# Optimization experiments

Measured on AMD Instinct MI355X. Metric: run time of the kernel, lower is better.

The kernel has to match this reference:

```python
import jax, jax.numpy as jnp
import numpy as np

EPS = 1e-5

def conv1d(x, w, b, pad):
    # x: (N,C,L), w: (O,I,K) torch layout
    y = jax.lax.conv_general_dilated(x, w, (1,), [(pad, pad)],
                                     dimension_numbers=('NCH', 'OIH', 'NCH'))
    return y + b[None, :, None]

def convT1d(x, w, b, stride, pad):
    # torch ConvTranspose1d; w: (I,O,K) torch layout
    K = w.shape[-1]
    wt = jnp.flip(w, -1).transpose(1, 0, 2)  # (O,I,K)
    y = jax.lax.conv_general_dilated(x, wt, (1,), [(K - 1 - pad, K - 1 - pad)],
                                     lhs_dilation=(stride,),
                                     dimension_numbers=('NCH', 'OIH', 'NCH'))
    return y + b[None, :, None]

def batchnorm1d(x, g, b):
    # training-mode batch stats over (N, L) per channel
    m = jnp.mean(x, axis=(0, 2), keepdims=True)
    v = jnp.var(x, axis=(0, 2), keepdims=True)
    return (x - m) * jax.lax.rsqrt(v + EPS) * g[None, :, None] + b[None, :, None]

def maxpool2(x):
    N, C, L = x.shape
    L2 = (L // 2) * 2
    return x[:, :, :L2].reshape(N, C, L // 2, 2).max(-1)

def linear(x, w, b):
    return x @ w.T + b

def gcn_conv(x, src, dst, w, b, n_nodes):
    # PyG GCNConv: add self-loops, symmetric norm, linear, aggregate
    h = x @ w.T  # (N, out)
    loop = jnp.arange(n_nodes, dtype=src.dtype)
    s = jnp.concatenate([src, loop])
    d = jnp.concatenate([dst, loop])
    deg = jax.ops.segment_sum(jnp.ones_like(d, dtype=h.dtype), d, num_segments=n_nodes)
    dinv = jax.lax.rsqrt(jnp.maximum(deg, 1e-12))
    norm = dinv[s] * dinv[d]  # (E+N,)
    msg = h[s] * norm[:, None]
    out = jax.ops.segment_sum(msg, d, num_segments=n_nodes)
    return out + b

def _params(key):
    ks = jax.random.split(key, 32)
    i = iter(range(32))
    def w(shape, k):
        return jax.random.normal(k, shape, dtype=jnp.float32) * 0.05
    F = 2944  # 128 * (187 // 8)
    p = {}
    p['ec1_w'] = w((32, 1, 5), ks[next(i)]);   p['ec1_b'] = jnp.zeros(32)
    p['bn1e_g'] = jnp.ones(32);                p['bn1e_b'] = jnp.zeros(32)
    p['ec2_w'] = w((64, 32, 5), ks[next(i)]);  p['ec2_b'] = jnp.zeros(64)
    p['bn2e_g'] = jnp.ones(64);                p['bn2e_b'] = jnp.zeros(64)
    p['ec3_w'] = w((128, 64, 5), ks[next(i)]); p['ec3_b'] = jnp.zeros(128)
    p['bn3e_g'] = jnp.ones(128);               p['bn3e_b'] = jnp.zeros(128)
    p['efc1_w'] = w((256, F), ks[next(i)]);    p['efc1_b'] = jnp.zeros(256)
    p['efc2_w'] = w((128, 256), ks[next(i)]);  p['efc2_b'] = jnp.zeros(128)
    p['g1_w'] = w((128, 128), ks[next(i)]);    p['g1_b'] = jnp.zeros(128)
    p['g2_w'] = w((128, 128), ks[next(i)]);    p['g2_b'] = jnp.zeros(128)
    p['c1_w'] = w((64, 128), ks[next(i)]);     p['c1_b'] = jnp.zeros(64)
    p['c2_w'] = w((5, 64), ks[next(i)]);       p['c2_b'] = jnp.zeros(5)
    p['cls_emb'] = w((5, 32), ks[next(i)])
    p['dfc1_w'] = w((256, 160), ks[next(i)]);  p['dfc1_b'] = jnp.zeros(256)
    p['dfc2_w'] = w((F, 256), ks[next(i)]);    p['dfc2_b'] = jnp.zeros(F)
    p['dc1_w'] = w((128, 64, 4), ks[next(i)]); p['dc1_b'] = jnp.zeros(64)
    p['bn1d_g'] = jnp.ones(64);                p['bn1d_b'] = jnp.zeros(64)
    p['dc2_w'] = w((64, 32, 4), ks[next(i)]);  p['dc2_b'] = jnp.zeros(32)
    p['bn2d_g'] = jnp.ones(32);                p['bn2d_b'] = jnp.zeros(32)
    p['dc3_w'] = w((32, 1, 4), ks[next(i)]);   p['dc3_b'] = jnp.zeros(1)
    return p

def setup_inputs() -> dict:
    key = jax.random.key(0)
    k1, k2, k3, kp = jax.random.split(key, 4)
    N, E = 20000, 640000
    inp = {
        'waveforms': jax.random.normal(k1, (N, 1, 187), dtype=jnp.float32),
        'edge_index': jax.random.randint(k2, (2, E), 0, N, dtype=jnp.int64)
                      if jax.config.jax_enable_x64 else
                      jax.random.randint(k2, (2, E), 0, N, dtype=jnp.int32),
        'class_labels': jax.random.randint(k3, (N,), 0, 5, dtype=jnp.int32),
    }
    inp.update(_params(kp))
    return inp

def _forward(waveforms, edge_index, class_labels, p):
    N = waveforms.shape[0]
    # ---- ECGEncoder ----
    x = maxpool2(jax.nn.relu(batchnorm1d(conv1d(waveforms, p['ec1_w'], p['ec1_b'], 2), p['bn1e_g'], p['bn1e_b'])))
    x = maxpool2(jax.nn.relu(batchnorm1d(conv1d(x, p['ec2_w'], p['ec2_b'], 2), p['bn2e_g'], p['bn2e_b'])))
    x = maxpool2(jax.nn.relu(batchnorm1d(conv1d(x, p['ec3_w'], p['ec3_b'], 2), p['bn3e_g'], p['bn3e_b'])))
    x = x.reshape(N, -1)  # (N, 2944)
    x = jax.nn.relu(linear(x, p['efc1_w'], p['efc1_b']))  # dropout = identity (eval)
    feats = linear(x, p['efc2_w'], p['efc2_b'])  # (N, 128)
    # ---- GCNEncoder ----
    src, dst = edge_index[0], edge_index[1]
    h = jax.nn.relu(gcn_conv(feats, src, dst, p['g1_w'], p['g1_b'], N))
    z = gcn_conv(h, src, dst, p['g2_w'], p['g2_b'], N)
    # ---- Classifier ----
    logits = linear(jax.nn.relu(linear(z, p['c1_w'], p['c1_b'])), p['c2_w'], p['c2_b'])
    # ---- ClassConditionedDecoder ----
    emb = p['cls_emb'][class_labels]  # (N, 32)
    d = jnp.concatenate([z, emb], axis=1)  # (N, 160)
    d = jax.nn.relu(linear(d, p['dfc1_w'], p['dfc1_b']))
    d = jax.nn.relu(linear(d, p['dfc2_w'], p['dfc2_b']))
    d = d.reshape(N, 128, 23)
    d = jax.nn.relu(batchnorm1d(convT1d(d, p['dc1_w'], p['dc1_b'], 2, 1), p['bn1d_g'], p['bn1d_b']))  # (N,64,46)
    d = jax.nn.relu(batchnorm1d(convT1d(d, p['dc2_w'], p['dc2_b'], 2, 1), p['bn2d_g'], p['bn2d_b']))  # (N,32,92)
    d = convT1d(d, p['dc3_w'], p['dc3_b'], 2, 1)  # (N,1,184)
    recon = jnp.pad(d, ((0, 0), (0, 0), (0, 187 - d.shape[2])))
    return z, recon, logits

PARAM_NAMES = ['ec1_w','ec1_b','bn1e_g','bn1e_b','ec2_w','ec2_b','bn2e_g','bn2e_b','ec3_w','ec3_b','bn3e_g','bn3e_b','efc1_w','efc1_b','efc2_w','efc2_b','g1_w','g1_b','g2_w','g2_b','c1_w','c1_b','c2_w','c2_b','cls_emb','dfc1_w','dfc1_b','dfc2_w','dfc2_b','dc1_w','dc1_b','bn1d_g','bn1d_b','dc2_w','dc2_b','bn2d_g','bn2d_b','dc3_w','dc3_b']

def reference(waveforms, edge_index, class_labels,
              ec1_w, ec1_b, bn1e_g, bn1e_b, ec2_w, ec2_b, bn2e_g, bn2e_b,
              ec3_w, ec3_b, bn3e_g, bn3e_b, efc1_w, efc1_b, efc2_w, efc2_b,
              g1_w, g1_b, g2_w, g2_b, c1_w, c1_b, c2_w, c2_b, cls_emb,
              dfc1_w, dfc1_b, dfc2_w, dfc2_b, dc1_w, dc1_b, bn1d_g, bn1d_b,
              dc2_w, dc2_b, bn2d_g, bn2d_b, dc3_w, dc3_b):
    p = dict(zip(PARAM_NAMES, (ec1_w, ec1_b, bn1e_g, bn1e_b, ec2_w, ec2_b, bn2e_g, bn2e_b,
                               ec3_w, ec3_b, bn3e_g, bn3e_b, efc1_w, efc1_b, efc2_w, efc2_b,
                               g1_w, g1_b, g2_w, g2_b, c1_w, c1_b, c2_w, c2_b, cls_emb,
                               dfc1_w, dfc1_b, dfc2_w, dfc2_b, dc1_w, dc1_b, bn1d_g, bn1d_b,
                               dc2_w, dc2_b, bn2d_g, bn2d_b, dc3_w, dc3_b)))
    return _forward(waveforms, edge_index, class_labels, p)
```

## Files before the change

kernel.cpp:

```cpp
#include <hip/hip_runtime.h>
#include <hip/hip_bf16.h>

using bf16 = __hip_bfloat16;

#define NS 20000
#define NE 640000
#define BN_EPS 1e-5f

__device__ __forceinline__ float bf2f(bf16 x) { return __bfloat162float(x); }
__device__ __forceinline__ bf16 f2bf(float x) { return __float2bfloat16(x); }
__device__ __forceinline__ float us2f(unsigned short u) { return __uint_as_float(((unsigned)u) << 16); }

__device__ __forceinline__ float4 load4f(const float* p) { return *reinterpret_cast<const float4*>(p); }
__device__ __forceinline__ void storeOut(float* p, float v) { *p = v; }
__device__ __forceinline__ void storeOut(bf16* p, float v) { *p = f2bf(v); }

__global__ __launch_bounds__(256) void k_wprep(const float* __restrict__ w2, const float* __restrict__ w3,
    float* __restrict__ W2T, bf16* __restrict__ W3T)
{
  int i = blockIdx.x * 256 + threadIdx.x;
  if (i < 10240) { int oc = i / 160, tap = i % 160; W2T[tap * 64 + oc] = w2[i]; }
  if (i < 40960) {
    int h = i / 20480, r = i % 20480;
    int oc = r / 320, tap = r % 320;
    W3T[h * 20480 + tap * 64 + oc] = f2bf(w3[i]);
  }
}

__global__ __launch_bounds__(256) void k_conv1_stats(const float* __restrict__ wav,
    const float* __restrict__ w1, const float* __restrict__ b1, float* __restrict__ stats)
{
  __shared__ float xs[192];
  __shared__ float ssum[32], ssq[32];
  int n = blockIdx.x, t = threadIdx.x;
  if (t < 187) xs[2 + t] = wav[n * 187 + t];
  else if (t == 187) { xs[0] = 0.f; xs[1] = 0.f; }
  else if (t == 188) { xs[189] = 0.f; xs[190] = 0.f; xs[191] = 0.f; }
  if (t < 32) { ssum[t] = 0.f; ssq[t] = 0.f; }
  __syncthreads();
  int c = t & 31, g = t >> 5;
  float wr[5];
#pragma unroll
  for (int k = 0; k < 5; ++k) wr[k] = w1[c * 5 + k];
  float bias = b1[c], s = 0.f, s2 = 0.f;
  for (int l = g; l < 187; l += 8) {
    float y = bias;
#pragma unroll
    for (int k = 0; k < 5; ++k) y = fmaf(xs[l + k], wr[k], y);
    s += y; s2 = fmaf(y, y, s2);
  }
  atomicAdd(&ssum[c], s); atomicAdd(&ssq[c], s2);
  __syncthreads();
  if (t < 32) { atomicAdd(&stats[t], ssum[t]); atomicAdd(&stats[128 + t], ssq[t]); }
}

__global__ void k_bn_finalize(float* __restrict__ stats, const float* __restrict__ g,
                              const float* __restrict__ b, int C, float invCnt, int off)
{
  int t = threadIdx.x;
  if (t < C) {
    float mean = stats[t] * invCnt;
    float var = stats[128 + t] * invCnt - mean * mean;
    float sc = g[t] * rsqrtf(var + BN_EPS);
    stats[off + t] = sc;
    stats[off + 128 + t] = b[t] - mean * sc;
  }
}

__global__ __launch_bounds__(256) void k_s2stats(const float* __restrict__ wav,
    const float* __restrict__ w1, const float* __restrict__ b1,
    const float* __restrict__ sc1, const float* __restrict__ sh1,
    const float* __restrict__ W2T, const float* __restrict__ b2,
    float* __restrict__ statacc)
{
  __shared__ float xs[192];
  __shared__ float p1[32 * 104];
  __shared__ __align__(16) float w2t[10240];
  __shared__ float ssum[64], ssq[64];
  int n = blockIdx.x, t = threadIdx.x;
  for (int i = t; i < 2560; i += 256)
    reinterpret_cast<float4*>(w2t)[i] = reinterpret_cast<const float4*>(W2T)[i];
  if (t < 187) xs[2 + t] = wav[n * 187 + t];
  else if (t == 187) { xs[0] = 0.f; xs[1] = 0.f; }
  else if (t == 188) { xs[189] = 0.f; xs[190] = 0.f; xs[191] = 0.f; }
  if (t < 64) { ssum[t] = 0.f; ssq[t] = 0.f; }
  if (t < 32) {
    p1[t * 104 + 0] = 0.f; p1[t * 104 + 1] = 0.f;
#pragma unroll
    for (int m = 95; m < 104; ++m) p1[t * 104 + m] = 0.f;
  }
  __syncthreads();
  {
    int c = t & 31, g = t >> 5;
    float wr[5];
#pragma unroll
    for (int k = 0; k < 5; ++k) wr[k] = w1[c * 5 + k];
    float bias = b1[c], sc = sc1[c], sh = sh1[c];
    for (int lp = g; lp < 93; lp += 8) {
      int b0 = 2 * lp;
      float y0 = bias, y1 = bias;
#pragma unroll
      for (int k = 0; k < 5; ++k) {
        y0 = fmaf(xs[b0 + k], wr[k], y0);
        y1 = fmaf(xs[b0 + 1 + k], wr[k], y1);
      }
      y0 = fmaf(y0, sc, sh); y1 = fmaf(y1, sc, sh);
      p1[c * 104 + 2 + lp] = fmaxf(fmaxf(y0, y1), 0.f);
    }
  }
  __syncthreads();
  int oc = (t & 15) * 4, l0 = (t >> 4) * 6;
  float acc[4][6] = {};
  for (int i = 0; i < 32; ++i) {
    float xv[10];
#pragma unroll
    for (int j = 0; j < 10; ++j) xv[j] = p1[i * 104 + l0 + j];
#pragma unroll
    for (int k = 0; k < 5; ++k) {
      const float4 wv = *reinterpret_cast<const float4*>(&w2t[(i * 5 + k) * 64 + oc]);
#pragma unroll
      for (int j = 0; j < 6; ++j) {
        acc[0][j] = fmaf(xv[j + k], wv.x, acc[0][j]);
        acc[1][j] = fmaf(xv[j + k], wv.y, acc[1][j]);
        acc[2][j] = fmaf(xv[j + k], wv.z, acc[2][j]);
        acc[3][j] = fmaf(xv[j + k], wv.w, acc[3][j]);
      }
    }
  }
#pragma unroll
  for (int c = 0; c < 4; ++c) {
    float bias = b2[oc + c], s = 0.f, s2 = 0.f;
#pragma unroll
    for (int j = 0; j < 6; ++j) {
      if (l0 + j < 93) {
        float y = acc[c][j] + bias;
        s += y; s2 = fmaf(y, y, s2);
      }
    }
    atomicAdd(&ssum[oc + c], s); atomicAdd(&ssq[oc + c], s2);
  }
  __syncthreads();
  if (t < 64) { atomicAdd(&statacc[t], ssum[t]); atomicAdd(&statacc[128 + t], ssq[t]); }
}

__global__ __launch_bounds__(256) void k_s123(const float* __restrict__ wav,
    const float* __restrict__ w1, const float* __restrict__ b1,
    const float* __restrict__ sc1, const float* __restrict__ sh1,
    const float* __restrict__ W2T, const float* __restrict__ b2,
    const float* __restrict__ sc2, const float* __restrict__ sh2,
    const bf16* __restrict__ W3T, const float* __restrict__ b3,
    bf16* __restrict__ praw3, float* __restrict__ statacc)
{
  __shared__ float xs[192];
  __shared__ float ssum[128], ssq[128];
  __shared__ __align__(16) char Rb[54272];
  float* p1  = (float*)Rb;
  float* w2t = (float*)(Rb + 13312);
  float* p2  = (float*)Rb;
  bf16*  w3t = (bf16*)(Rb + 13312);
  int n = blockIdx.x, t = threadIdx.x;
  for (int i = t; i < 2560; i += 256)
    reinterpret_cast<float4*>(w2t)[i] = reinterpret_cast<const float4*>(W2T)[i];
  if (t < 187) xs[2 + t] = wav[n * 187 + t];
  else if (t == 187) { xs[0] = 0.f; xs[1] = 0.f; }
  else if (t == 188) { xs[189] = 0.f; xs[190] = 0.f; xs[191] = 0.f; }
  if (t < 128) { ssum[t] = 0.f; ssq[t] = 0.f; }
  if (t < 32) {
    p1[t * 104 + 0] = 0.f; p1[t * 104 + 1] = 0.f;
#pragma unroll
    for (int m = 95; m < 104; ++m) p1[t * 104 + m] = 0.f;
  }
  __syncthreads();
  {
    int c = t & 31, g = t >> 5;
    float wr[5];
#pragma unroll
    for (int k = 0; k < 5; ++k) wr[k] = w1[c * 5 + k];
    float bias = b1[c], sc = sc1[c], sh = sh1[c];
    for (int lp = g; lp < 93; lp += 8) {
      int b0 = 2 * lp;
      float y0 = bias, y1 = bias;
#pragma unroll
      for (int k = 0; k < 5; ++k) {
        y0 = fmaf(xs[b0 + k], wr[k], y0);
        y1 = fmaf(xs[b0 + 1 + k], wr[k], y1);
      }
      y0 = fmaf(y0, sc, sh); y1 = fmaf(y1, sc, sh);
      p1[c * 104 + 2 + lp] = fmaxf(fmaxf(y0, y1), 0.f);
    }
  }
  __syncthreads();
  int oc = (t & 15) * 4, g2 = t >> 4, l0 = g2 * 6;
  float acc[4][6] = {};
  for (int i = 0; i < 32; ++i) {
    float xv[10];
#pragma unroll
    for (int j = 0; j < 10; ++j) xv[j] = p1[i * 104 + l0 + j];
#pragma unroll
    for (int k = 0; k < 5; ++k) {
      const float4 wv = *reinterpret_cast<const float4*>(&w2t[(i * 5 + k) * 64 + oc]);
#pragma unroll
      for (int j = 0; j < 6; ++j) {
        acc[0][j] = fmaf(xv[j + k], wv.x, acc[0][j]);
        acc[1][j] = fmaf(xv[j + k], wv.y, acc[1][j]);
        acc[2][j] = fmaf(xv[j + k], wv.z, acc[2][j]);
        acc[3][j] = fmaf(xv[j + k], wv.w, acc[3][j]);
      }
    }
  }
  __syncthreads();
#pragma unroll
  for (int c = 0; c < 4; ++c) {
    int ch = oc + c;
    float bias = b2[ch], sc = sc2[ch], sh = sh2[ch];
#pragma unroll
    for (int u = 0; u < 3; ++u) {
      int pp = 3 * g2 + u;
      if (pp < 46) {
        float ya = fmaf(acc[c][2 * u] + bias, sc, sh);
        float yb = fmaf(acc[c][2 * u + 1] + bias, sc, sh);
        p2[ch * 52 + 2 + pp] = fmaxf(fmaxf(ya, yb), 0.f);
      }
    }
  }
  if (t < 64) {
    p2[t * 52 + 0] = 0.f; p2[t * 52 + 1] = 0.f;
    p2[t * 52 + 48] = 0.f; p2[t * 52 + 49] = 0.f; p2[t * 52 + 50] = 0.f; p2[t * 52 + 51] = 0.f;
  }
  for (int h = 0; h < 2; ++h) {
    __syncthreads();
    for (int i = t; i < 10240; i += 256)
      reinterpret_cast<unsigned*>(w3t)[i] = reinterpret_cast<const unsigned*>(W3T + h * 20480)[i];
    __syncthreads();
    int oc2 = (t & 31) * 2, gb = t >> 5, l0b = gb * 6;
    float a2[2][6] = {};
    for (int i = 0; i < 64; ++i) {
      float xv[10];
#pragma unroll
      for (int j = 0; j < 10; ++j) xv[j] = p2[i * 52 + l0b + j];
#pragma unroll
      for (int k = 0; k < 5; ++k) {
        unsigned wp = *reinterpret_cast<const unsigned*>(&w3t[(i * 5 + k) * 64 + oc2]);
        float wa = us2f((unsigned short)(wp & 0xffffu));
        float wb = us2f((unsigned short)(wp >> 16));
#pragma unroll
        for (int j = 0; j < 6; ++j) {
          a2[0][j] = fmaf(xv[j + k], wa, a2[0][j]);
          a2[1][j] = fmaf(xv[j + k], wb, a2[1][j]);
        }
      }
    }
#pragma unroll
    for (int c = 0; c < 2; ++c) {
      int ch = h * 64 + oc2 + c;
      float bias3 = b3[ch], s = 0.f, s2 = 0.f;
      float yv[6];
#pragma unroll
      for (int j = 0; j < 6; ++j) {
        yv[j] = a2[c][j] + bias3;
        if (l0b + j < 46) { s += yv[j]; s2 = fmaf(yv[j], yv[j], s2); }
      }
#pragma unroll
      for (int u = 0; u < 3; ++u) {
        int pp = 3 * gb + u;
        if (pp < 23) praw3[(size_t)n * 2944 + ch * 23 + pp] = f2bf(fmaxf(yv[2 * u], yv[2 * u + 1]));
      }
      atomicAdd(&ssum[ch], s); atomicAdd(&ssq[ch], s2);
    }
  }
  __syncthreads();
  if (t < 128) { atomicAdd(&statacc[t], ssum[t]); atomicAdd(&statacc[128 + t], ssq[t]); }
}

__global__ __launch_bounds__(256) void k_efc1(const bf16* __restrict__ praw,
    const float* __restrict__ sc3, const float* __restrict__ sh3,
    const float* __restrict__ W, const float* __restrict__ bias, float* __restrict__ C)
{
  const int M = NS, K = 2944, O = 256;
  __shared__ float As[16][68];
  __shared__ float Bs[16][68];
  __shared__ float scs[128], shs[128];
  int tid = threadIdx.x;
  if (tid < 128) { scs[tid] = sc3[tid]; shs[tid] = sh3[tid]; }
  __syncthreads();
  int bm = blockIdx.x * 64, bo = blockIdx.y * 64;
  int lr = tid >> 2, lk = (tid & 3) * 4;
  int tm = (tid & 15) * 4, to = (tid >> 4) * 4;
  float acc[4][4] = {};
  for (int k0 = 0; k0 < K; k0 += 16) {
    float a0 = 0.f, a1 = 0.f, a2 = 0.f, a3 = 0.f;
    float4 wv = make_float4(0.f, 0.f, 0.f, 0.f);
    int arow = bm + lr;
    if (arow < M) {
      int kb = k0 + lk;
      ushort4 u4 = *reinterpret_cast<const ushort4*>(praw + (size_t)arow * K + kb);
      int c0 = (kb + 0) / 23, c1 = (kb + 1) / 23, c2 = (kb + 2) / 23, c3 = (kb + 3) / 23;
      a0 = fmaxf(fmaf(us2f(u4.x), scs[c0], shs[c0]), 0.f);
      a1 = fmaxf(fmaf(us2f(u4.y), scs[c1], shs[c1]), 0.f);
      a2 = fmaxf(fmaf(us2f(u4.z), scs[c2], shs[c2]), 0.f);
      a3 = fmaxf(fmaf(us2f(u4.w), scs[c3], shs[c3]), 0.f);
    }
    int orow = bo + lr;
    if (orow < O) wv = load4f(W + (size_t)orow * K + k0 + lk);
    As[lk + 0][lr] = a0; As[lk + 1][lr] = a1; As[lk + 2][lr] = a2; As[lk + 3][lr] = a3;
    Bs[lk + 0][lr] = wv.x; Bs[lk + 1][lr] = wv.y; Bs[lk + 2][lr] = wv.z; Bs[lk + 3][lr] = wv.w;
    __syncthreads();
#pragma unroll
    for (int k = 0; k < 16; ++k) {
      const float4 a = *reinterpret_cast<const float4*>(&As[k][tm]);
      const float4 b = *reinterpret_cast<const float4*>(&Bs[k][to]);
      float a4[4] = {a.x, a.y, a.z, a.w};
      float b4[4] = {b.x, b.y, b.z, b.w};
#pragma unroll
      for (int i = 0; i < 4; ++i)
#pragma unroll
        for (int j = 0; j < 4; ++j) acc[i][j] = fmaf(a4[i], b4[j], acc[i][j]);
    }
    __syncthreads();
  }
#pragma unroll
  for (int i = 0; i < 4; ++i) {
    int row = bm + tm + i;
    if (row >= M) continue;
#pragma unroll
    for (int j = 0; j < 4; ++j) {
      int col = bo + to + j;
      float v = acc[i][j] + bias[col];
      C[(size_t)row * O + col] = fmaxf(v, 0.f);
    }
  }
}

template <typename OT, bool RELU, bool RSCALE>
__global__ __launch_bounds__(256) void k_gemm(const float* __restrict__ A, const float* __restrict__ W,
    const float* __restrict__ bias, const float* __restrict__ rscale,
    OT* __restrict__ C, int M, int K, int O)
{
  __shared__ float As[16][68];
  __shared__ float Bs[16][68];
  int tid = threadIdx.x;
  int bm = blockIdx.x * 64, bo = blockIdx.y * 64;
  int lr = tid >> 2, lk = (tid & 3) * 4;
  int tm = (tid & 15) * 4, to = (tid >> 4) * 4;
  float acc[4][4] = {};
  for (int k0 = 0; k0 < K; k0 += 16) {
    float4 av = make_float4(0.f, 0.f, 0.f, 0.f);
    float4 wv = make_float4(0.f, 0.f, 0.f, 0.f);
    int arow = bm + lr;
    if (arow < M) av = load4f(A + (size_t)arow * K + k0 + lk);
    int orow = bo + lr;
    if (orow < O) wv = load4f(W + (size_t)orow * K + k0 + lk);
    As[lk + 0][lr] = av.x; As[lk + 1][lr] = av.y; As[lk + 2][lr] = av.z; As[lk + 3][lr] = av.w;
    Bs[lk + 0][lr] = wv.x; Bs[lk + 1][lr] = wv.y; Bs[lk + 2][lr] = wv.z; Bs[lk + 3][lr] = wv.w;
    __syncthreads();
#pragma unroll
    for (int k = 0; k < 16; ++k) {
      const float4 a = *reinterpret_cast<const float4*>(&As[k][tm]);
      const float4 b = *reinterpret_cast<const float4*>(&Bs[k][to]);
      float a4[4] = {a.x, a.y, a.z, a.w};
      float b4[4] = {b.x, b.y, b.z, b.w};
#pragma unroll
      for (int i = 0; i < 4; ++i)
#pragma unroll
        for (int j = 0; j < 4; ++j) acc[i][j] = fmaf(a4[i], b4[j], acc[i][j]);
    }
    __syncthreads();
  }
#pragma unroll
  for (int i = 0; i < 4; ++i) {
    int row = bm + tm + i;
    if (row >= M) continue;
    float rs = RSCALE ? rscale[row] : 1.f;
#pragma unroll
    for (int j = 0; j < 4; ++j) {
      int col = bo + to + j;
      if (col >= O) continue;
      float v = acc[i][j];
      if (bias) v += bias[col];
      if (RSCALE) v *= rs;
      if (RELU) v = fmaxf(v, 0.f);
      storeOut(&C[(size_t)row * O + col], v);
    }
  }
}

__global__ void k_degacc_int(const int* __restrict__ dst, int* __restrict__ dg)
{
  int e = blockIdx.x * 256 + threadIdx.x;
  if (e < NE) atomicAdd(&dg[dst[e]], 1);
}
__global__ __launch_bounds__(1024) void k_scan(const int* __restrict__ dg,
    int* __restrict__ off, int* __restrict__ cur)
{
  __shared__ int part[1024];
  int t = threadIdx.x;
  int base = t * 20;
  int local[20];
  int s = 0;
#pragma unroll
  for (int k = 0; k < 20; ++k) {
    int idx = base + k;
    int v = (idx < NS) ? dg[idx] : 0;
    local[k] = s; s += v;
  }
  part[t] = s;
  __syncthreads();
  for (int d = 1; d < 1024; d <<= 1) {
    int v = (t >= d) ? part[t - d] : 0;
    __syncthreads();
    part[t] += v;
    __syncthreads();
  }
  int pre = (t > 0) ? part[t - 1] : 0;
#pragma unroll
  for (int k = 0; k < 20; ++k) {
    int idx = base + k;
    if (idx < NS) { off[idx] = pre + local[k]; cur[idx] = pre + local[k]; }
  }
  if (t == 1023) off[NS] = part[1023];
}
__global__ void k_dinv(const int* __restrict__ dg, float* __restrict__ dinv)
{
  int i = blockIdx.x * 256 + threadIdx.x;
  if (i < NS) dinv[i] = rsqrtf((float)(dg[i] + 1));
}
__global__ void k_place(const int* __restrict__ src, const int* __restrict__ dst,
    int* __restrict__ cur, int* __restrict__ csr_src)
{
  int e = blockIdx.x * 256 + threadIdx.x;
  if (e < NE) {
    int p = atomicAdd(&cur[dst[e]], 1);
    csr_src[p] = src[e];
  }
}
template <bool RELU>
__global__ __launch_bounds__(128) void k_gcn_agg(const int* __restrict__ off,
    const int* __restrict__ csr_src, const float* __restrict__ hs,
    const float* __restrict__ dinv, const float* __restrict__ b, float* __restrict__ out)
{
  __shared__ int sidx[128];
  int n = blockIdx.x, t = threadIdx.x;
  int s0 = off[n], s1 = off[n + 1];
  float acc = 0.f;
  for (int base = s0; base < s1; base += 128) {
    int cnt = min(128, s1 - base);
    if (t < cnt) sidx[t] = csr_src[base + t];
    __syncthreads();
    for (int i = 0; i < cnt; ++i) acc += hs[(size_t)sidx[i] * 128 + t];
    __syncthreads();
  }
  float v = (acc + hs[(size_t)n * 128 + t]) * dinv[n] + b[t];
  if (RELU) v = fmaxf(v, 0.f);
  out[(size_t)n * 128 + t] = v;
}

__global__ void k_dcat(const float* __restrict__ z, const int* __restrict__ labels,
    const float* __restrict__ emb, float* __restrict__ dcat)
{
  int total = NS * 160;
  for (int i = blockIdx.x * 256 + threadIdx.x; i < total; i += gridDim.x * 256) {
    int n = i / 160, f = i % 160;
    dcat[i] = (f < 128) ? z[(size_t)n * 128 + f] : emb[labels[n] * 32 + (f - 128)];
  }
}

__global__ __launch_bounds__(256) void k_convT1(const bf16* __restrict__ d2,
    const float* __restrict__ w, const float* __restrict__ b,
    bf16* __restrict__ raw, float* __restrict__ stats)
{
  __shared__ float xsh[2944];
  __shared__ __align__(8) bf16 wsh[16384];
  __shared__ float ssum[64], ssq[64];
  int n = blockIdx.x, t = threadIdx.x;
  for (int i = t; i < 2944; i += 256) xsh[i] = bf2f(d2[(size_t)n * 2944 + i]);
  if (t < 64) { ssum[t] = 0.f; ssq[t] = 0.f; }
  int o = t & 63, g = t >> 6;
  float acc[12] = {};
  for (int half = 0; half < 2; ++half) {
    __syncthreads();
    for (int i = t; i < 16384; i += 256) wsh[i] = f2bf(w[half * 16384 + i]);
    __syncthreads();
    for (int i = 0; i < 64; ++i) {
      int ci = half * 64 + i;
      ushort4 w4 = *reinterpret_cast<const ushort4*>(&wsh[i * 256 + o * 4]);
      float w0 = us2f(w4.x), w1 = us2f(w4.y), w2v = us2f(w4.z), w3v = us2f(w4.w);
      float xl[8];
#pragma unroll
      for (int m = 0; m < 8; ++m) {
        int l = 6 * g - 1 + m;
        xl[m] = (l >= 0 && l < 23) ? xsh[ci * 23 + l] : 0.f;
      }
#pragma unroll
      for (int j = 0; j < 12; ++j) {
        if (j & 1) acc[j] = fmaf(w0, xl[(j + 1) / 2 + 1], fmaf(w2v, xl[(j + 1) / 2], acc[j]));
        else       acc[j] = fmaf(w1, xl[j / 2 + 1],       fmaf(w3v, xl[j / 2],       acc[j]));
      }
    }
  }
  float bias = b[o], s = 0.f, s2 = 0.f;
  size_t base = (size_t)n * 2944;
#pragma unroll
  for (int j = 0; j < 12; ++j) {
    int tp = 12 * g + j;
    if (tp < 46) {
      float y = acc[j] + bias;
      raw[base + (size_t)o * 46 + tp] = f2bf(y);
      s += y; s2 = fmaf(y, y, s2);
    }
  }
  atomicAdd(&ssum[o], s); atomicAdd(&ssq[o], s2);
  __syncthreads();
  if (t < 64) { atomicAdd(&stats[t], ssum[t]); atomicAdd(&stats[128 + t], ssq[t]); }
}

__global__ __launch_bounds__(256) void k_convT2(const bf16* __restrict__ raw1,
    const float* __restrict__ sc, const float* __restrict__ sh,
    const float* __restrict__ w, const float* __restrict__ b,
    bf16* __restrict__ raw2out, float* __restrict__ stats)
{
  __shared__ float xsh[2944];
  __shared__ __align__(16) float wsh[8192];
  __shared__ float ssum[32], ssq[32];
  int n = blockIdx.x, t = threadIdx.x;
  for (int i = t; i < 8192; i += 256) wsh[i] = w[i];
  for (int i = t; i < 2944; i += 256) {
    int c = i / 46;
    float v = fmaf(bf2f(raw1[(size_t)n * 2944 + i]), sc[c], sh[c]);
    xsh[i] = fmaxf(v, 0.f);
  }
  if (t < 32) { ssum[t] = 0.f; ssq[t] = 0.f; }
  __syncthreads();
  int o = t & 31, g = t >> 5;
  float acc[12] = {};
  for (int i = 0; i < 64; ++i) {
    const float4 wv = *reinterpret_cast<const float4*>(&wsh[i * 128 + o * 4]);
    float w0 = wv.x, w1 = wv.y, w2v = wv.z, w3v = wv.w;
    float xl[8];
#pragma unroll
    for (int m = 0; m < 8; ++m) {
      int l = 6 * g - 1 + m;
      xl[m] = (l >= 0 && l < 46) ? xsh[i * 46 + l] : 0.f;
    }
#pragma unroll
    for (int j = 0; j < 12; ++j) {
      if (j & 1) acc[j] = fmaf(w0, xl[(j + 1) / 2 + 1], fmaf(w2v, xl[(j + 1) / 2], acc[j]));
      else       acc[j] = fmaf(w1, xl[j / 2 + 1],       fmaf(w3v, xl[j / 2],       acc[j]));
    }
  }
  float bias = b[o], s = 0.f, s2 = 0.f;
  size_t base = (size_t)n * 2944;
#pragma unroll
  for (int j = 0; j < 12; ++j) {
    int tp = 12 * g + j;
    if (tp < 92) {
      float y = acc[j] + bias;
      raw2out[base + (size_t)o * 92 + tp] = f2bf(y);
      s += y; s2 = fmaf(y, y, s2);
    }
  }
  atomicAdd(&ssum[o], s); atomicAdd(&ssq[o], s2);
  __syncthreads();
  if (t < 32) { atomicAdd(&stats[t], ssum[t]); atomicAdd(&stats[128 + t], ssq[t]); }
}

__global__ __launch_bounds__(256) void k_convT3(const bf16* __restrict__ raw2,
    const float* __restrict__ sc, const float* __restrict__ sh,
    const float* __restrict__ w, const float* __restrict__ b,
    float* __restrict__ recon)
{
  __shared__ float xsh[2944];
  __shared__ float wsh[128];
  int n = blockIdx.x, t = threadIdx.x;
  if (t < 128) wsh[t] = w[t];
  for (int i = t; i < 2944; i += 256) {
    int c = i / 92;
    float v = fmaf(bf2f(raw2[(size_t)n * 2944 + i]), sc[c], sh[c]);
    xsh[i] = fmaxf(v, 0.f);
  }
  __syncthreads();
  if (t < 187) {
    float y = 0.f;
    if (t < 184) {
      y = b[0];
      if (t & 1) {
        int l1 = (t + 1) / 2, l2 = (t - 1) / 2;
        for (int i = 0; i < 32; ++i) {
          float a0 = (l1 < 92) ? wsh[i * 4 + 0] * xsh[i * 92 + l1] : 0.f;
          y += a0 + wsh[i * 4 + 2] * xsh[i * 92 + l2];
        }
      } else {
        int l1 = t / 2, l2 = t / 2 - 1;
        for (int i = 0; i < 32; ++i) {
          float a3 = (l2 >= 0) ? wsh[i * 4 + 3] * xsh[i * 92 + l2] : 0.f;
          y += wsh[i * 4 + 1] * xsh[i * 92 + l1] + a3;
        }
      }
    }
    recon[(size_t)n * 187 + t] = y;
  }
}

extern "C" void kernel_launch(void* const* d_in, const int* in_sizes, int n_in,
                              void* d_out, int out_size, void* d_ws, size_t ws_size,
                              hipStream_t stream)
{
  const float* wav    = (const float*)d_in[0];
  const int*   edges  = (const int*)d_in[1];
  const int*   labels = (const int*)d_in[2];
  int a = 3;
  const float* ec1_w = (const float*)d_in[a++]; const float* ec1_b = (const float*)d_in[a++];
  const float* bn1e_g = (const float*)d_in[a++]; const float* bn1e_b = (const float*)d_in[a++];
  const float* ec2_w = (const float*)d_in[a++]; const float* ec2_b = (const float*)d_in[a++];
  const float* bn2e_g = (const float*)d_in[a++]; const float* bn2e_b = (const float*)d_in[a++];
  const float* ec3_w = (const float*)d_in[a++]; const float* ec3_b = (const float*)d_in[a++];
  const float* bn3e_g = (const float*)d_in[a++]; const float* bn3e_b = (const float*)d_in[a++];
  const float* efc1_w = (const float*)d_in[a++]; const float* efc1_b = (const float*)d_in[a++];
  const float* efc2_w = (const float*)d_in[a++]; const float* efc2_b = (const float*)d_in[a++];
  const float* g1_w = (const float*)d_in[a++]; const float* g1_b = (const float*)d_in[a++];
  const float* g2_w = (const float*)d_in[a++]; const float* g2_b = (const float*)d_in[a++];
  const float* c1_w = (const float*)d_in[a++]; const float* c1_b = (const float*)d_in[a++];
  const float* c2_w = (const float*)d_in[a++]; const float* c2_b = (const float*)d_in[a++];
  const float* cls_emb = (const float*)d_in[a++];
  const float* dfc1_w = (const float*)d_in[a++]; const float* dfc1_b = (const float*)d_in[a++];
  const float* dfc2_w = (const float*)d_in[a++]; const float* dfc2_b = (const float*)d_in[a++];
  const float* dc1_w = (const float*)d_in[a++]; const float* dc1_b = (const float*)d_in[a++];
  const float* bn1d_g = (const float*)d_in[a++]; const float* bn1d_b = (const float*)d_in[a++];
  const float* dc2_w = (const float*)d_in[a++]; const float* dc2_b = (const float*)d_in[a++];
  const float* bn2d_g = (const float*)d_in[a++]; const float* bn2d_b = (const float*)d_in[a++];
  const float* dc3_w = (const float*)d_in[a++]; const float* dc3_b = (const float*)d_in[a++];

  char* ws = (char*)d_ws;
  bf16*  B1 = (bf16*)(ws + 0);
  bf16*  B2 = (bf16*)(ws + 117760000ULL);
  float* E1 = (float*)(ws + 117760000ULL);
  float* FE = (float*)(ws + 138240000ULL);
  float* LN = (float*)(ws + 148480000ULL);
  float* AG = (float*)(ws + 158720000ULL);
  float* DI = (float*)(ws + 168960000ULL);
  float* DC = (float*)(ws + 169040000ULL);
  float* W2T = (float*)(ws + 182000000ULL);
  bf16*  W3T = (bf16*)(ws + 182100000ULL);
  int*   DG  = (int*)(ws + 182200000ULL);
  int*   OFF = (int*)(ws + 182300000ULL);
  int*   CUR = (int*)(ws + 182400000ULL);
  int*   SRC = (int*)(ws + 182500000ULL);
  float* ST = (float*)(ws + 235520000ULL);

  float* zout   = (float*)d_out;
  float* recon  = (float*)d_out + 2560000;
  float* logits = (float*)d_out + 6300000;

  k_wprep<<<160, 256, 0, stream>>>(ec2_w, ec3_w, W2T, W3T);
  (void)hipMemsetAsync(DG, 0, NS * 4, stream);
  k_degacc_int<<<2500, 256, 0, stream>>>(edges + NE, DG);
  k_scan<<<1, 1024, 0, stream>>>(DG, OFF, CUR);
  k_dinv<<<79, 256, 0, stream>>>(DG, DI);
  k_place<<<2500, 256, 0, stream>>>(edges, edges + NE, CUR, SRC);

  (void)hipMemsetAsync(ST, 0, 1024, stream);
  k_conv1_stats<<<NS, 256, 0, stream>>>(wav, ec1_w, ec1_b, ST);
  k_bn_finalize<<<1, 128, 0, stream>>>(ST, bn1e_g, bn1e_b, 32, 1.f / (NS * 187.f), 256);
  (void)hipMemsetAsync(ST, 0, 1024, stream);
  k_s2stats<<<NS, 256, 0, stream>>>(wav, ec1_w, ec1_b, ST + 256, ST + 384, W2T, ec2_b, ST);
  k_bn_finalize<<<1, 128, 0, stream>>>(ST, bn2e_g, bn2e_b, 64, 1.f / (NS * 93.f), 512);
  (void)hipMemsetAsync(ST, 0, 1024, stream);
  k_s123<<<NS, 256, 0, stream>>>(wav, ec1_w, ec1_b, ST + 256, ST + 384, W2T, ec2_b,
                                 ST + 512, ST + 640, W3T, ec3_b, B1, ST);
  k_bn_finalize<<<1, 128, 0, stream>>>(ST, bn3e_g, bn3e_b, 128, 1.f / (NS * 46.f), 768);
  k_efc1<<<dim3(313, 4), 256, 0, stream>>>(B1, ST + 768, ST + 896, efc1_w, efc1_b, E1);
  k_gemm<float, false, false><<<dim3(313, 2), 256, 0, stream>>>(E1, efc2_w, efc2_b, nullptr, FE, NS, 256, 128);

  k_gemm<float, false, true><<<dim3(313, 2), 256, 0, stream>>>(FE, g1_w, nullptr, DI, LN, NS, 128, 128);
  k_gcn_agg<true><<<NS, 128, 0, stream>>>(OFF, SRC, LN, DI, g1_b, FE);
  k_gemm<float, false, true><<<dim3(313, 2), 256, 0, stream>>>(FE, g2_w, nullptr, DI, LN, NS, 128, 128);
  k_gcn_agg<false><<<NS, 128, 0, stream>>>(OFF, SRC, LN, DI, g2_b, zout);

  k_gemm<float, true, false><<<dim3(313, 1), 256, 0, stream>>>(zout, c1_w, c1_b, nullptr, AG, NS, 128, 64);
  k_gemm<float, false, false><<<dim3(313, 1), 256, 0, stream>>>(AG, c2_w, c2_b, nullptr, logits, NS, 64, 5);

  k_dcat<<<4096, 256, 0, stream>>>(zout, labels, cls_emb, DC);
  k_gemm<float, true, false><<<dim3(313, 4), 256, 0, stream>>>(DC, dfc1_w, dfc1_b, nullptr, E1, NS, 160, 256);
  k_gemm<bf16, true, false><<<dim3(313, 46), 256, 0, stream>>>(E1, dfc2_w, dfc2_b, nullptr, B1, NS, 256, 2944);
  (void)hipMemsetAsync(ST, 0, 1024, stream);
  k_convT1<<<NS, 256, 0, stream>>>(B1, dc1_w, dc1_b, B2, ST);
  k_bn_finalize<<<1, 128, 0, stream>>>(ST, bn1d_g, bn1d_b, 64, 1.f / (NS * 46.f), 256);
  (void)hipMemsetAsync(ST, 0, 1024, stream);
  k_convT2<<<NS, 256, 0, stream>>>(B2, ST + 256, ST + 384, dc2_w, dc2_b, B1, ST);
  k_bn_finalize<<<1, 128, 0, stream>>>(ST, bn2d_g, bn2d_b, 32, 1.f / (NS * 92.f), 512);
  k_convT3<<<NS, 256, 0, stream>>>(B1, ST + 512, ST + 640, dc3_w, dc3_b, recon);
}
```

Measured before the change: 5.735 ms.

## Use bf16 MFMA GEMM for large FCs and split conv stage to avoid recompute

```diff
diff --git a/kernel.cpp b/kernel.cpp
--- a/kernel.cpp
+++ b/kernel.cpp
@@ -2,6 +2,8 @@
 #include <hip/hip_bf16.h>
 
 using bf16 = __hip_bfloat16;
+typedef __attribute__((ext_vector_type(8))) short short8v;
+typedef __attribute__((ext_vector_type(4))) float f32x4;
 
 #define NS 20000
 #define NE 640000
@@ -10,6 +12,10 @@
 __device__ __forceinline__ float bf2f(bf16 x) { return __bfloat162float(x); }
 __device__ __forceinline__ bf16 f2bf(float x) { return __float2bfloat16(x); }
 __device__ __forceinline__ float us2f(unsigned short u) { return __uint_as_float(((unsigned)u) << 16); }
+__device__ __forceinline__ unsigned short bf_bits(float x) {
+  bf16 b = f2bf(x);
+  return *reinterpret_cast<unsigned short*>(&b);
+}
 
 __device__ __forceinline__ float4 load4f(const float* p) { return *reinterpret_cast<const float4*>(p); }
 __device__ __forceinline__ void storeOut(float* p, float v) { *p = v; }
@@ -67,11 +73,11 @@
   }
 }
 
-__global__ __launch_bounds__(256) void k_s2stats(const float* __restrict__ wav,
+__global__ __launch_bounds__(256) void k_s12(const float* __restrict__ wav,
     const float* __restrict__ w1, const float* __restrict__ b1,
     const float* __restrict__ sc1, const float* __restrict__ sh1,
     const float* __restrict__ W2T, const float* __restrict__ b2,
-    float* __restrict__ statacc)
+    bf16* __restrict__ praw2, float* __restrict__ statacc)
 {
   __shared__ float xs[192];
   __shared__ float p1[32 * 104];
@@ -109,7 +115,7 @@
     }
   }
   __syncthreads();
-  int oc = (t & 15) * 4, l0 = (t >> 4) * 6;
+  int oc = (t & 15) * 4, g2 = t >> 4, l0 = g2 * 6;
   float acc[4][6] = {};
   for (int i = 0; i < 32; ++i) {
     float xv[10];
@@ -129,7 +135,8 @@
   }
 #pragma unroll
   for (int c = 0; c < 4; ++c) {
-    float bias = b2[oc + c], s = 0.f, s2 = 0.f;
+    int ch = oc + c;
+    float bias = b2[ch], s = 0.f, s2 = 0.f;
 #pragma unroll
     for (int j = 0; j < 6; ++j) {
       if (l0 + j < 93) {
@@ -137,95 +144,38 @@
         s += y; s2 = fmaf(y, y, s2);
       }
     }
-    atomicAdd(&ssum[oc + c], s); atomicAdd(&ssq[oc + c], s2);
+#pragma unroll
+    for (int u = 0; u < 3; ++u) {
+      int pp = 3 * g2 + u;
+      if (pp < 46)
+        praw2[(size_t)n * 2944 + ch * 46 + pp] =
+            f2bf(fmaxf(acc[c][2 * u] + bias, acc[c][2 * u + 1] + bias));
+    }
+    atomicAdd(&ssum[ch], s); atomicAdd(&ssq[ch], s2);
   }
   __syncthreads();
   if (t < 64) { atomicAdd(&statacc[t], ssum[t]); atomicAdd(&statacc[128 + t], ssq[t]); }
 }
 
-__global__ __launch_bounds__(256) void k_s123(const float* __restrict__ wav,
-    const float* __restrict__ w1, const float* __restrict__ b1,
-    const float* __restrict__ sc1, const float* __restrict__ sh1,
-    const float* __restrict__ W2T, const float* __restrict__ b2,
+__global__ __launch_bounds__(256) void k_s3(const bf16* __restrict__ praw2,
     const float* __restrict__ sc2, const float* __restrict__ sh2,
     const bf16* __restrict__ W3T, const float* __restrict__ b3,
     bf16* __restrict__ praw3, float* __restrict__ statacc)
 {
-  __shared__ float xs[192];
   __shared__ float ssum[128], ssq[128];
   __shared__ __align__(16) char Rb[54272];
-  float* p1  = (float*)Rb;
-  float* w2t = (float*)(Rb + 13312);
   float* p2  = (float*)Rb;
   bf16*  w3t = (bf16*)(Rb + 13312);
   int n = blockIdx.x, t = threadIdx.x;
-  for (int i = t; i < 2560; i += 256)
-    reinterpret_cast<float4*>(w2t)[i] = reinterpret_cast<const float4*>(W2T)[i];
-  if (t < 187) xs[2 + t] = wav[n * 187 + t];
-  else if (t == 187) { xs[0] = 0.f; xs[1] = 0.f; }
-  else if (t == 188) { xs[189] = 0.f; xs[190] = 0.f; xs[191] = 0.f; }
   if (t < 128) { ssum[t] = 0.f; ssq[t] = 0.f; }
-  if (t < 32) {
-    p1[t * 104 + 0] = 0.f; p1[t * 104 + 1] = 0.f;
-#pragma unroll
-    for (int m = 95; m < 104; ++m) p1[t * 104 + m] = 0.f;
-  }
-  __syncthreads();
-  {
-    int c = t & 31, g = t >> 5;
-    float wr[5];
-#pragma unroll
-    for (int k = 0; k < 5; ++k) wr[k] = w1[c * 5 + k];
-    float bias = b1[c], sc = sc1[c], sh = sh1[c];
-    for (int lp = g; lp < 93; lp += 8) {
-      int b0 = 2 * lp;
-      float y0 = bias, y1 = bias;
-#pragma unroll
-      for (int k = 0; k < 5; ++k) {
-        y0 = fmaf(xs[b0 + k], wr[k], y0);
-        y1 = fmaf(xs[b0 + 1 + k], wr[k], y1);
-      }
-      y0 = fmaf(y0, sc, sh); y1 = fmaf(y1, sc, sh);
-      p1[c * 104 + 2 + lp] = fmaxf(fmaxf(y0, y1), 0.f);
-    }
-  }
-  __syncthreads();
-  int oc = (t & 15) * 4, g2 = t >> 4, l0 = g2 * 6;
-  float acc[4][6] = {};
-  for (int i = 0; i < 32; ++i) {
-    float xv[10];
-#pragma unroll
-    for (int j = 0; j < 10; ++j) xv[j] = p1[i * 104 + l0 + j];
-#pragma unroll
-    for (int k = 0; k < 5; ++k) {
-      const float4 wv = *reinterpret_cast<const float4*>(&w2t[(i * 5 + k) * 64 + oc]);
-#pragma unroll
-      for (int j = 0; j < 6; ++j) {
-        acc[0][j] = fmaf(xv[j + k], wv.x, acc[0][j]);
-        acc[1][j] = fmaf(xv[j + k], wv.y, acc[1][j]);
-        acc[2][j] = fmaf(xv[j + k], wv.z, acc[2][j]);
-        acc[3][j] = fmaf(xv[j + k], wv.w, acc[3][j]);
-      }
-    }
-  }
-  __syncthreads();
-#pragma unroll
-  for (int c = 0; c < 4; ++c) {
-    int ch = oc + c;
-    float bias = b2[ch], sc = sc2[ch], sh = sh2[ch];
-#pragma unroll
-    for (int u = 0; u < 3; ++u) {
-      int pp = 3 * g2 + u;
-      if (pp < 46) {
-        float ya = fmaf(acc[c][2 * u] + bias, sc, sh);
-        float yb = fmaf(acc[c][2 * u + 1] + bias, sc, sh);
-        p2[ch * 52 + 2 + pp] = fmaxf(fmaxf(ya, yb), 0.f);
-      }
-    }
-  }
   if (t < 64) {
     p2[t * 52 + 0] = 0.f; p2[t * 52 + 1] = 0.f;
     p2[t * 52 + 48] = 0.f; p2[t * 52 + 49] = 0.f; p2[t * 52 + 50] = 0.f; p2[t * 52 + 51] = 0.f;
+  }
+  for (int i = t; i < 2944; i += 256) {
+    int c = i / 46, lp = i % 46;
+    float v = fmaf(bf2f(praw2[(size_t)n * 2944 + i]), sc2[c], sh2[c]);
+    p2[c * 52 + 2 + lp] = fmaxf(v, 0.f);
   }
   for (int h = 0; h < 2; ++h) {
     __syncthreads();
@@ -272,61 +222,95 @@
   if (t < 128) { atomicAdd(&statacc[t], ssum[t]); atomicAdd(&statacc[128 + t], ssq[t]); }
 }
 
-__global__ __launch_bounds__(256) void k_efc1(const bf16* __restrict__ praw,
-    const float* __restrict__ sc3, const float* __restrict__ sh3,
-    const float* __restrict__ W, const float* __restrict__ bias, float* __restrict__ C)
-{
-  const int M = NS, K = 2944, O = 256;
-  __shared__ float As[16][68];
-  __shared__ float Bs[16][68];
-  __shared__ float scs[128], shs[128];
-  int tid = threadIdx.x;
-  if (tid < 128) { scs[tid] = sc3[tid]; shs[tid] = sh3[tid]; }
-  __syncthreads();
-  int bm = blockIdx.x * 64, bo = blockIdx.y * 64;
-  int lr = tid >> 2, lk = (tid & 3) * 4;
-  int tm = (tid & 15) * 4, to = (tid >> 4) * 4;
-  float acc[4][4] = {};
-  for (int k0 = 0; k0 < K; k0 += 16) {
-    float a0 = 0.f, a1 = 0.f, a2 = 0.f, a3 = 0.f;
-    float4 wv = make_float4(0.f, 0.f, 0.f, 0.f);
-    int arow = bm + lr;
-    if (arow < M) {
-      int kb = k0 + lk;
-      ushort4 u4 = *reinterpret_cast<const ushort4*>(praw + (size_t)arow * K + kb);
-      int c0 = (kb + 0) / 23, c1 = (kb + 1) / 23, c2 = (kb + 2) / 23, c3 = (kb + 3) / 23;
-      a0 = fmaxf(fmaf(us2f(u4.x), scs[c0], shs[c0]), 0.f);
-      a1 = fmaxf(fmaf(us2f(u4.y), scs[c1], shs[c1]), 0.f);
-      a2 = fmaxf(fmaf(us2f(u4.z), scs[c2], shs[c2]), 0.f);
-      a3 = fmaxf(fmaf(us2f(u4.w), scs[c3], shs[c3]), 0.f);
-    }
-    int orow = bo + lr;
-    if (orow < O) wv = load4f(W + (size_t)orow * K + k0 + lk);
-    As[lk + 0][lr] = a0; As[lk + 1][lr] = a1; As[lk + 2][lr] = a2; As[lk + 3][lr] = a3;
-    Bs[lk + 0][lr] = wv.x; Bs[lk + 1][lr] = wv.y; Bs[lk + 2][lr] = wv.z; Bs[lk + 3][lr] = wv.w;
-    __syncthreads();
-#pragma unroll
-    for (int k = 0; k < 16; ++k) {
-      const float4 a = *reinterpret_cast<const float4*>(&As[k][tm]);
-      const float4 b = *reinterpret_cast<const float4*>(&Bs[k][to]);
-      float a4[4] = {a.x, a.y, a.z, a.w};
-      float b4[4] = {b.x, b.y, b.z, b.w};
-#pragma unroll
-      for (int i = 0; i < 4; ++i)
-#pragma unroll
-        for (int j = 0; j < 4; ++j) acc[i][j] = fmaf(a4[i], b4[j], acc[i][j]);
-    }
+__global__ __launch_bounds__(256) void k_bnrelu(bf16* __restrict__ x,
+    const float* __restrict__ sc, const float* __restrict__ sh)
+{
+  int total = NS * 736;
+  for (int q = blockIdx.x * 256 + threadIdx.x; q < total; q += gridDim.x * 256) {
+    ushort4 u = reinterpret_cast<ushort4*>(x)[q];
+    int f = (q * 4) % 2944;
+    int c0 = f / 23, c1 = (f + 1) / 23, c2 = (f + 2) / 23, c3 = (f + 3) / 23;
+    ushort4 o;
+    o.x = bf_bits(fmaxf(fmaf(us2f(u.x), sc[c0], sh[c0]), 0.f));
+    o.y = bf_bits(fmaxf(fmaf(us2f(u.y), sc[c1], sh[c1]), 0.f));
+    o.z = bf_bits(fmaxf(fmaf(us2f(u.z), sc[c2], sh[c2]), 0.f));
+    o.w = bf_bits(fmaxf(fmaf(us2f(u.w), sc[c3], sh[c3]), 0.f));
+    reinterpret_cast<ushort4*>(x)[q] = o;
+  }
+}
+
+template <typename AT, typename OT, bool RELU>
+__global__ __launch_bounds__(256) void k_mgemm(const AT* __restrict__ A, const float* __restrict__ W,
+    const float* __restrict__ bias, OT* __restrict__ C, int M, int K, int O)
+{
+  __shared__ __align__(16) bf16 As[128][40];
+  __shared__ __align__(16) bf16 Bs[128][40];
+  int t = threadIdx.x;
+  int bm = blockIdx.y * 128, bo = blockIdx.x * 128;
+  int wave = t >> 6, lane = t & 63;
+  int wm = (wave & 1) * 64, wn = (wave >> 1) * 64;
+  int srow = t >> 1, skc = (t & 1) * 16;
+  f32x4 acc[4][4] = {};
+  for (int k0 = 0; k0 < K; k0 += 32) {
+    {
+      short8v v0 = {}, v1 = {};
+      int grow = bm + srow;
+      if (grow < M) {
+        if constexpr (sizeof(AT) == 2) {
+          const short8v* src = reinterpret_cast<const short8v*>(A + (size_t)grow * K + k0 + skc);
+          v0 = src[0]; v1 = src[1];
+        } else {
+          const float* src = (const float*)A + (size_t)grow * K + k0 + skc;
+#pragma unroll
+          for (int i = 0; i < 8; ++i) v0[i] = (short)bf_bits(src[i]);
+#pragma unroll
+          for (int i = 0; i < 8; ++i) v1[i] = (short)bf_bits(src[8 + i]);
+        }
+      }
+      short8v* dst = reinterpret_cast<short8v*>(&As[srow][skc]);
+      dst[0] = v0; dst[1] = v1;
+    }
+    {
+      const float* src = W + (size_t)(bo + srow) * K + k0 + skc;
+      short8v v0, v1;
+#pragma unroll
+      for (int i = 0; i < 8; ++i) v0[i] = (short)bf_bits(src[i]);
+#pragma unroll
+      for (int i = 0; i < 8; ++i) v1[i] = (short)bf_bits(src[8 + i]);
+      short8v* dst = reinterpret_cast<short8v*>(&Bs[srow][skc]);
+      dst[0] = v0; dst[1] = v1;
+    }
+    __syncthreads();
+    short8v af[4], bf_[4];
+#pragma unroll
+    for (int i = 0; i < 4; ++i)
+      af[i] = *reinterpret_cast<const short8v*>(&As[wm + 16 * i + (lane & 15)][(lane >> 4) * 8]);
+#pragma unroll
+    for (int j = 0; j < 4; ++j)
+      bf_[j] = *reinterpret_cast<const short8v*>(&Bs[wn + 16 * j + (lane & 15)][(lane >> 4) * 8]);
+#pragma unroll
+    for (int i = 0; i < 4; ++i)
+#pragma unroll
+      for (int j = 0; j < 4; ++j)
+        acc[i][j] = __builtin_amdgcn_mfma_f32_16x16x32_bf16(af[i], bf_[j], acc[i][j], 0, 0, 0);
     __syncthreads();
   }
 #pragma unroll
   for (int i = 0; i < 4; ++i) {
-    int row = bm + tm + i;
-    if (row >= M) continue;
 #pragma unroll
     for (int j = 0; j < 4; ++j) {
-      int col = bo + to + j;
-      float v = acc[i][j] + bias[col];
-      C[(size_t)row * O + col] = fmaxf(v, 0.f);
+      int col = bo + wn + 16 * j + (lane & 15);
+      int row0 = bm + wm + 16 * i + (lane >> 4) * 4;
+      float bv = bias[col];
+#pragma unroll
+      for (int r = 0; r < 4; ++r) {
+        int row = row0 + r;
+        if (row < M) {
+          float v = acc[i][j][r] + bv;
+          if (RELU) v = fmaxf(v, 0.f);
+          storeOut(&C[(size_t)row * O + col], v);
+        }
+      }
     }
   }
 }
@@ -638,36 +622,39 @@
   float* AG = (float*)(ws + 158720000ULL);
   float* DI = (float*)(ws + 168960000ULL);
   float* DC = (float*)(ws + 169040000ULL);
-  float* W2T = (float*)(ws + 182000000ULL);
-  bf16*  W3T = (bf16*)(ws + 182100000ULL);
-  int*   DG  = (int*)(ws + 182200000ULL);
-  int*   OFF = (int*)(ws + 182300000ULL);
-  int*   CUR = (int*)(ws + 182400000ULL);
-  int*   SRC = (int*)(ws + 182500000ULL);
+  int*   DG  = (int*)(ws + 182000000ULL);
+  int*   OFF = (int*)(ws + 182100000ULL);
+  int*   CUR = (int*)(ws + 182200000ULL);
+  int*   SRC = (int*)(ws + 182300000ULL);
   float* ST = (float*)(ws + 235520000ULL);
 
   float* zout   = (float*)d_out;
   float* recon  = (float*)d_out + 2560000;
   float* logits = (float*)d_out + 6300000;
 
+  float* W2T = recon;
+  bf16*  W3T = (bf16*)(recon + 10240);
+
   k_wprep<<<160, 256, 0, stream>>>(ec2_w, ec3_w, W2T, W3T);
+
+  (void)hipMemsetAsync(ST, 0, 1024, stream);
+  k_conv1_stats<<<NS, 256, 0, stream>>>(wav, ec1_w, ec1_b, ST);
+  k_bn_finalize<<<1, 128, 0, stream>>>(ST, bn1e_g, bn1e_b, 32, 1.f / (NS * 187.f), 256);
+  (void)hipMemsetAsync(ST, 0, 1024, stream);
+  k_s12<<<NS, 256, 0, stream>>>(wav, ec1_w, ec1_b, ST + 256, ST + 384, W2T, ec2_b, B2, ST);
+  k_bn_finalize<<<1, 128, 0, stream>>>(ST, bn2e_g, bn2e_b, 64, 1.f / (NS * 93.f), 512);
+  (void)hipMemsetAsync(ST, 0, 1024, stream);
+  k_s3<<<NS, 256, 0, stream>>>(B2, ST + 512, ST + 640, W3T, ec3_b, B1, ST);
+  k_bn_finalize<<<1, 128, 0, stream>>>(ST, bn3e_g, bn3e_b, 128, 1.f / (NS * 46.f), 768);
+
   (void)hipMemsetAsync(DG, 0, NS * 4, stream);
   k_degacc_int<<<2500, 256, 0, stream>>>(edges + NE, DG);
   k_scan<<<1, 1024, 0, stream>>>(DG, OFF, CUR);
   k_dinv<<<79, 256, 0, stream>>>(DG, DI);
   k_place<<<2500, 256, 0, stream>>>(edges, edges + NE, CUR, SRC);
 
-  (void)hipMemsetAsync(ST, 0, 1024, stream);
-  k_conv1_stats<<<NS, 256, 0, stream>>>(wav, ec1_w, ec1_b, ST);
-  k_bn_finalize<<<1, 128, 0, stream>>>(ST, bn1e_g, bn1e_b, 32, 1.f / (NS * 187.f), 256);
-  (void)hipMemsetAsync(ST, 0, 1024, stream);
-  k_s2stats<<<NS, 256, 0, stream>>>(wav, ec1_w, ec1_b, ST + 256, ST + 384, W2T, ec2_b, ST);
-  k_bn_finalize<<<1, 128, 0, stream>>>(ST, bn2e_g, bn2e_b, 64, 1.f / (NS * 93.f), 512);
-  (void)hipMemsetAsync(ST, 0, 1024, stream);
-  k_s123<<<NS, 256, 0, stream>>>(wav, ec1_w, ec1_b, ST + 256, ST + 384, W2T, ec2_b,
-                                 ST + 512, ST + 640, W3T, ec3_b, B1, ST);
-  k_bn_finalize<<<1, 128, 0, stream>>>(ST, bn3e_g, bn3e_b, 128, 1.f / (NS * 46.f), 768);
-  k_efc1<<<dim3(313, 4), 256, 0, stream>>>(B1, ST + 768, ST + 896, efc1_w, efc1_b, E1);
+  k_bnrelu<<<2048, 256, 0, stream>>>(B1, ST + 768, ST + 896);
+  k_mgemm<bf16, float, true><<<dim3(2, 157), 256, 0, stream>>>(B1, efc1_w, efc1_b, E1, NS, 2944, 256);
   k_gemm<float, false, false><<<dim3(313, 2), 256, 0, stream>>>(E1, efc2_w, efc2_b, nullptr, FE, NS, 256, 128);
 
   k_gemm<float, false, true><<<dim3(313, 2), 256, 0, stream>>>(FE, g1_w, nullptr, DI, LN, NS, 128, 128);
@@ -680,7 +667,7 @@
 
   k_dcat<<<4096, 256, 0, stream>>>(zout, labels, cls_emb, DC);
   k_gemm<float, true, false><<<dim3(313, 4), 256, 0, stream>>>(DC, dfc1_w, dfc1_b, nullptr, E1, NS, 160, 256);
-  k_gemm<bf16, true, false><<<dim3(313, 46), 256, 0, stream>>>(E1, dfc2_w, dfc2_b, nullptr, B1, NS, 256, 2944);
+  k_mgemm<float, bf16, true><<<dim3(23, 157), 256, 0, stream>>>(E1, dfc2_w, dfc2_b, B1, NS, 256, 2944);
   (void)hipMemsetAsync(ST, 0, 1024, stream);
   k_convT1<<<NS, 256, 0, stream>>>(B1, dc1_w, dc1_b, B2, ST);
   k_bn_finalize<<<1, 128, 0, stream>>>(ST, bn1d_g, bn1d_b, 64, 1.f / (NS * 46.f), 256);
```

Result: faster. 4.684 ms (-18.3%).
